# Optimization experiments

Measured on AMD Instinct MI355X. Metric: run time of the kernel, lower is better.

The kernel has to match this reference:

```python
import jax, jax.numpy as jnp
import numpy as np

EPS = 1e-5
R = 3


def _layernorm(x, gamma, beta):
    mu = jnp.mean(x, axis=-1, keepdims=True)
    var = jnp.mean(jnp.square(x - mu), axis=-1, keepdims=True)
    return (x - mu) * jax.lax.rsqrt(var + EPS) * gamma + beta


def setup_inputs() -> dict:
    key = jax.random.key(0)
    ks = jax.random.split(key, 16)
    N, C, H, W = 32, 256, 32, 32
    ic = C // 2
    L = H * W
    R2 = R * R
    d_attn = R2 * L        # 9216
    d_out = ic * L         # 131072
    return {
        "x": jax.random.normal(ks[0], (N, C, H, W), jnp.float32),
        "wq": jax.random.normal(ks[1], (ic, C), jnp.float32) / np.sqrt(C),
        "wk": jax.random.normal(ks[2], (ic, C), jnp.float32) / np.sqrt(C),
        "gamma1": jnp.ones((d_attn,), jnp.float32),
        "beta1": jnp.zeros((d_attn,), jnp.float32),
        "w1": jax.random.normal(ks[3], (C, d_attn), jnp.float32) / np.sqrt(d_attn),
        "b1": jnp.zeros((C,), jnp.float32),
        "w2": jax.random.normal(ks[4], (d_out, C), jnp.float32) / np.sqrt(C),
        "b2": jnp.zeros((d_out,), jnp.float32),
        "gamma2": jnp.ones((d_out,), jnp.float32),
        "beta2": jnp.zeros((d_out,), jnp.float32),
        "w_out": jax.random.normal(ks[5], (C, ic), jnp.float32) / np.sqrt(ic),
        "bn_gamma": jax.random.normal(ks[6], (C,), jnp.float32),
        "bn_beta": jax.random.normal(ks[7], (C,), jnp.float32),
        "bn_mean": jax.random.normal(ks[8], (C,), jnp.float32),
        "bn_var": jax.random.uniform(ks[9], (C,), jnp.float32, 0.5, 1.5),
    }


def reference(x, wq, wk, gamma1, beta1, w1, b1, w2, b2, gamma2, beta2,
              w_out, bn_gamma, bn_beta, bn_mean, bn_var):
    N, C, H, W = x.shape
    ic = wq.shape[0]
    L = H * W
    R2 = R * R
    pad = (R - 1) // 2

    # 1x1 convs == channel GEMMs
    q = jnp.einsum('nchw,oc->nohw', x, wq).reshape(N, ic, L)       # [N,ic,L]
    k = jnp.einsum('nchw,oc->nohw', x, wk)                          # [N,ic,H,W]

    # unfold: RxR local patches, torch channel-major ordering [ic, R2]
    kp = jnp.pad(k, ((0, 0), (0, 0), (pad, pad), (pad, pad)))
    patches = jnp.stack([kp[:, :, i:i + H, j:j + W]
                         for i in range(R) for j in range(R)], axis=-1)
    patches = patches.reshape(N, ic, L, R2)                         # [N,ic,L,R2]

    # local attention scores: q . k over channels at each spatial loc
    f = jnp.einsum('ncl,nclr->nlr', q, patches)                     # [N,L,R2]
    f = f.transpose(0, 2, 1).reshape(N, R2 * L)                     # [N, R2*L]

    # f = f + dropout(f) -> identity at inference => 2f
    f = f + f
    f = _layernorm(f, gamma1, beta1)

    # FFN
    h = jax.nn.relu(f @ w1.T + b1)                                  # [N,C]
    h = h @ w2.T + b2                                               # [N, ic*L]
    h = _layernorm(h, gamma2, beta2)
    y = h.reshape(N, ic, H, W)

    # output 1x1 conv + BatchNorm2d (inference mode)
    wy = jnp.einsum('nchw,oc->nohw', y, w_out)                      # [N,C,H,W]
    scale = (bn_gamma * jax.lax.rsqrt(bn_var + EPS))[None, :, None, None]
    wy = (wy - bn_mean[None, :, None, None]) * scale + bn_beta[None, :, None, None]
    return wy + x
```

## Files before the change

kernel.cpp:

```cpp
#include <hip/hip_runtime.h>

#define NN 32
#define CC 256
#define LL 1024
#define IC 128
#define R2 9
#define DA 9216
#define DOUT 131072
#define EPSF 1e-5f

typedef __attribute__((ext_vector_type(8))) short short8;
typedef __attribute__((ext_vector_type(4))) float f32x4;

__device__ __forceinline__ ushort bf_rne(float f) {
  union { float f; unsigned u; } v;
  v.f = f;
  unsigned u = v.u;
  u += 0x7FFF + ((u >> 16) & 1);
  return (ushort)(u >> 16);
}

__global__ __launch_bounds__(256) void k_xt(const float* __restrict__ x,
                                            ushort* __restrict__ xt) {
  int n = blockIdx.y;
  int l = blockIdx.x * 128 + (threadIdx.x & 127);
  int chalf = (threadIdx.x >> 7) * 128;
  const float* xn = x + ((size_t)n * CC) * LL;
  ushort* xr = xt + ((size_t)n * LL + l) * CC + chalf;
#pragma unroll 4
  for (int c4 = 0; c4 < 32; c4++) {
    float a = xn[(size_t)(chalf + c4 * 4 + 0) * LL + l];
    float b = xn[(size_t)(chalf + c4 * 4 + 1) * LL + l];
    float c = xn[(size_t)(chalf + c4 * 4 + 2) * LL + l];
    float d = xn[(size_t)(chalf + c4 * 4 + 3) * LL + l];
    ushort4 o;
    o.x = bf_rne(a); o.y = bf_rne(b); o.z = bf_rne(c); o.w = bf_rne(d);
    *(ushort4*)(xr + c4 * 4) = o;
  }
}

__global__ __launch_bounds__(256, 1) void k_qk(const ushort* __restrict__ xt,
                                               const float* __restrict__ wq,
                                               const float* __restrict__ wk,
                                               float* __restrict__ q,
                                               float* __restrict__ k) {
  int bx = blockIdx.x;
  int n = blockIdx.y;
  int mt = bx & 1, lt = bx >> 1;
  int l0 = lt * 256;
  int t = threadIdx.x;
  int lane = t & 63, wv = t >> 6;
  int m16 = lane & 15, kg = lane >> 4;
  const float* wrow = mt ? wk : wq;

  short8 a[2][8];
#pragma unroll
  for (int ms = 0; ms < 2; ms++)
#pragma unroll
    for (int kc = 0; kc < 8; kc++) {
      const float* ap =
          wrow + (size_t)(wv * 32 + ms * 16 + m16) * CC + kc * 32 + kg * 8;
      short8 v;
#pragma unroll
      for (int j = 0; j < 8; j++) v[j] = (short)bf_rne(ap[j]);
      a[ms][kc] = v;
    }

  f32x4 acc0[16], acc1[16];
#pragma unroll
  for (int i = 0; i < 16; i++) {
    acc0[i] = (f32x4){0.f, 0.f, 0.f, 0.f};
    acc1[i] = (f32x4){0.f, 0.f, 0.f, 0.f};
  }

  const ushort* xrow = xt + ((size_t)n * LL + l0 + m16) * CC + kg * 8;
#pragma unroll
  for (int kc = 0; kc < 8; kc++) {
#pragma unroll
    for (int ls = 0; ls < 16; ls++) {
      short8 b = *(const short8*)(xrow + (size_t)ls * 16 * CC + kc * 32);
      acc0[ls] =
          __builtin_amdgcn_mfma_f32_16x16x32_bf16(a[0][kc], b, acc0[ls], 0, 0, 0);
      acc1[ls] =
          __builtin_amdgcn_mfma_f32_16x16x32_bf16(a[1][kc], b, acc1[ls], 0, 0, 0);
    }
  }

  float* outp = (mt ? k : q) + (size_t)n * IC * LL;
  int mq = kg * 4;
#pragma unroll
  for (int ls = 0; ls < 16; ls++) {
    int col = l0 + ls * 16 + m16;
#pragma unroll
    for (int r = 0; r < 4; r++) {
      outp[(size_t)(wv * 32 + mq + r) * LL + col] = acc0[ls][r];
      outp[(size_t)(wv * 32 + 16 + mq + r) * LL + col] = acc1[ls][r];
    }
  }
}

__global__ __launch_bounds__(256) void k_attn(const float* __restrict__ q,
                                              const float* __restrict__ k,
                                              float* __restrict__ f2) {
  int n = blockIdx.x;
  int c0 = blockIdx.y * 32;
  int l = blockIdx.z * 256 + threadIdx.x;
  int h = l >> 5, w = l & 31;
  const float* qn = q + (size_t)n * IC * LL;
  const float* kn = k + (size_t)n * IC * LL;
  bool val[9];
  int off[9];
#pragma unroll
  for (int i = 0; i < 3; i++)
#pragma unroll
    for (int j = 0; j < 3; j++) {
      int r = i * 3 + j;
      int hh = h + i - 1, ww = w + j - 1;
      val[r] = (hh >= 0 && hh < 32 && ww >= 0 && ww < 32);
      off[r] = hh * 32 + ww;
    }
  float acc[9];
#pragma unroll
  for (int r = 0; r < 9; r++) acc[r] = 0.f;
#pragma unroll 4
  for (int cc = 0; cc < 32; cc++) {
    int c = c0 + cc;
    float qv = qn[c * LL + l];
    const float* kc = kn + c * LL;
#pragma unroll
    for (int r = 0; r < 9; r++) {
      float kv = val[r] ? kc[off[r]] : 0.f;
      acc[r] += qv * kv;
    }
  }
#pragma unroll
  for (int r = 0; r < 9; r++)
    atomicAdd(&f2[(size_t)n * DA + r * LL + l], 2.f * acc[r]);
}

__global__ __launch_bounds__(256) void k_ln1(float* __restrict__ f2,
                                             const float* __restrict__ g1,
                                             const float* __restrict__ b1) {
  int n = blockIdx.x, t = threadIdx.x;
  float* row = f2 + (size_t)n * DA;
  float4 v[9];
  float s = 0.f, ss = 0.f;
#pragma unroll
  for (int kk = 0; kk < 9; kk++) {
    v[kk] = ((const float4*)row)[t + kk * 256];
    s += v[kk].x + v[kk].y + v[kk].z + v[kk].w;
    ss += v[kk].x * v[kk].x + v[kk].y * v[kk].y + v[kk].z * v[kk].z +
          v[kk].w * v[kk].w;
  }
#pragma unroll
  for (int o = 32; o; o >>= 1) {
    s += __shfl_down(s, o);
    ss += __shfl_down(ss, o);
  }
  __shared__ float ps[4], pss[4], stats[2];
  int wid = t >> 6, lid = t & 63;
  if (lid == 0) { ps[wid] = s; pss[wid] = ss; }
  __syncthreads();
  if (t == 0) {
    float S = ps[0] + ps[1] + ps[2] + ps[3];
    float SS = pss[0] + pss[1] + pss[2] + pss[3];
    float mu = S / DA;
    float var = SS / DA - mu * mu;
    stats[0] = mu;
    stats[1] = rsqrtf(var + EPSF);
  }
  __syncthreads();
  float mu = stats[0], rs = stats[1];
#pragma unroll
  for (int kk = 0; kk < 9; kk++) {
    float4 g = ((const float4*)g1)[t + kk * 256];
    float4 b = ((const float4*)b1)[t + kk * 256];
    float4 o;
    o.x = (v[kk].x - mu) * rs * g.x + b.x;
    o.y = (v[kk].y - mu) * rs * g.y + b.y;
    o.z = (v[kk].z - mu) * rs * g.z + b.z;
    o.w = (v[kk].w - mu) * rs * g.w + b.w;
    ((float4*)row)[t + kk * 256] = o;
  }
}

__global__ __launch_bounds__(256) void k_ffn1(const float* __restrict__ fln,
                                              const float* __restrict__ w1,
                                              const float* __restrict__ b1,
                                              ushort* __restrict__ h1bf) {
  int o = blockIdx.x, nsb = blockIdx.y * 8, t = threadIdx.x;
  float acc[8];
#pragma unroll
  for (int i = 0; i < 8; i++) acc[i] = 0.f;
  const float4* w1r = (const float4*)(w1 + (size_t)o * DA);
  for (int kk = 0; kk < 9; kk++) {
    float4 wv = w1r[t + kk * 256];
#pragma unroll
    for (int i = 0; i < 8; i++) {
      float4 fv = ((const float4*)(fln + (size_t)(nsb + i) * DA))[t + kk * 256];
      acc[i] += wv.x * fv.x + wv.y * fv.y + wv.z * fv.z + wv.w * fv.w;
    }
  }
#pragma unroll
  for (int i = 0; i < 8; i++)
#pragma unroll
    for (int s = 32; s; s >>= 1) acc[i] += __shfl_down(acc[i], s);
  __shared__ float part[4][8];
  int wid = t >> 6, lid = t & 63;
  if (lid == 0) {
#pragma unroll
    for (int i = 0; i < 8; i++) part[wid][i] = acc[i];
  }
  __syncthreads();
  if (t < 8) {
    float sum = part[0][t] + part[1][t] + part[2][t] + part[3][t] + b1[o];
    h1bf[(size_t)(nsb + t) * CC + o] = bf_rne(fmaxf(sum, 0.f));
  }
}

__global__ __launch_bounds__(256, 3) void k_ffn2(
    const ushort* __restrict__ h1bf, const float* __restrict__ w2,
    const float* __restrict__ b2, float* __restrict__ h2,
    float* __restrict__ st_part) {
  __shared__ float bs[64];
  int t = threadIdx.x;
  int lane = t & 63, wv = t >> 6;
  int m16 = lane & 15, kg = lane >> 4;
  int j0 = blockIdx.x * 256 + wv * 64;
  if (t < 64) bs[t] = 0.f;

  short8 a[2][8];
#pragma unroll
  for (int m = 0; m < 2; m++)
#pragma unroll
    for (int kc = 0; kc < 8; kc++)
      a[m][kc] = *(const short8*)(h1bf + (size_t)(m * 16 + m16) * CC +
                                  kc * 32 + kg * 8);

  f32x4 acc[2][4];
#pragma unroll
  for (int m = 0; m < 2; m++)
#pragma unroll
    for (int n = 0; n < 4; n++) acc[m][n] = (f32x4){0.f, 0.f, 0.f, 0.f};

  int j[4];
#pragma unroll
  for (int n = 0; n < 4; n++) j[n] = j0 + n * 16 + m16;

#pragma unroll
  for (int kc = 0; kc < 8; kc++) {
    short8 bfrag[4];
#pragma unroll
    for (int n = 0; n < 4; n++) {
      const float* src = w2 + (size_t)j[n] * CC + kc * 32 + kg * 8;
      float4 lo = *(const float4*)src;
      float4 hi = *(const float4*)(src + 4);
      union { short8 s; ushort u[8]; } cv;
      cv.u[0] = bf_rne(lo.x); cv.u[1] = bf_rne(lo.y);
      cv.u[2] = bf_rne(lo.z); cv.u[3] = bf_rne(lo.w);
      cv.u[4] = bf_rne(hi.x); cv.u[5] = bf_rne(hi.y);
      cv.u[6] = bf_rne(hi.z); cv.u[7] = bf_rne(hi.w);
      bfrag[n] = cv.s;
    }
#pragma unroll
    for (int m = 0; m < 2; m++)
#pragma unroll
      for (int n = 0; n < 4; n++)
        acc[m][n] = __builtin_amdgcn_mfma_f32_16x16x32_bf16(a[m][kc], bfrag[n],
                                                            acc[m][n], 0, 0, 0);
  }
  __syncthreads();

  float b2v[4];
#pragma unroll
  for (int n = 0; n < 4; n++) b2v[n] = b2[j[n]];

  float s8[2][4], q8[2][4];
#pragma unroll
  for (int m = 0; m < 2; m++)
#pragma unroll
    for (int r = 0; r < 4; r++) { s8[m][r] = 0.f; q8[m][r] = 0.f; }
#pragma unroll
  for (int m = 0; m < 2; m++)
#pragma unroll
    for (int n = 0; n < 4; n++) {
#pragma unroll
      for (int r = 0; r < 4; r++) {
        float v = acc[m][n][r] + b2v[n];
        int row = m * 16 + kg * 4 + r;
        h2[(size_t)row * DOUT + j[n]] = v;
        s8[m][r] += v;
        q8[m][r] += v * v;
      }
    }
#pragma unroll
  for (int off = 8; off; off >>= 1)
#pragma unroll
    for (int m = 0; m < 2; m++)
#pragma unroll
      for (int r = 0; r < 4; r++) {
        s8[m][r] += __shfl_down(s8[m][r], off, 16);
        q8[m][r] += __shfl_down(q8[m][r], off, 16);
      }
  if (m16 == 0) {
#pragma unroll
    for (int m = 0; m < 2; m++)
#pragma unroll
      for (int r = 0; r < 4; r++) {
        int row = m * 16 + kg * 4 + r;
        atomicAdd(&bs[row], s8[m][r]);
        atomicAdd(&bs[32 + row], q8[m][r]);
      }
  }
  __syncthreads();
  if (t < 64) st_part[(size_t)blockIdx.x * 64 + t] = bs[t];
}

__global__ __launch_bounds__(256) void k_stat(const float* __restrict__ st_part,
                                              float* __restrict__ st) {
  int e = blockIdx.x;
  int t = threadIdx.x;
  float s = 0.f;
  for (int p = t; p < 512; p += 256) s += st_part[(size_t)p * 64 + e];
#pragma unroll
  for (int off = 32; off; off >>= 1) s += __shfl_down(s, off);
  __shared__ float ps[4];
  if ((t & 63) == 0) ps[t >> 6] = s;
  __syncthreads();
  if (t == 0) st[e] = ps[0] + ps[1] + ps[2] + ps[3];
}

__global__ __launch_bounds__(256) void k_out(
    const float* __restrict__ h2, const float* __restrict__ st,
    const float* __restrict__ g2, const float* __restrict__ b2,
    const float* __restrict__ w_out, const float* __restrict__ bn_g,
    const float* __restrict__ bn_b, const float* __restrict__ bn_m,
    const float* __restrict__ bn_v, const float* __restrict__ x,
    float* __restrict__ out) {
  __shared__ float wt[IC * 32];
  __shared__ float yt[16 * 256];
  int t = threadIdx.x;
  int l0 = blockIdx.x * 256;
  int Ob = blockIdx.y * 32;
  int n = blockIdx.z;
  for (int f = t; f < IC * 32; f += 256) {
    int Os = f & 31, o = f >> 5;
    wt[o * 32 + Os] = w_out[(size_t)(Ob + Os) * IC + o];
  }
  float mu = st[n] * (1.f / DOUT);
  float rs = rsqrtf(st[32 + n] * (1.f / DOUT) - mu * mu + EPSF);
  int lane = t & 63, wid = t >> 6;
  int Obase = wid * 8;
  int ll = lane * 4;
  float4 acc[8];
#pragma unroll
  for (int i = 0; i < 8; i++) acc[i] = make_float4(0.f, 0.f, 0.f, 0.f);

  for (int o0 = 0; o0 < IC; o0 += 16) {
    __syncthreads();
#pragma unroll
    for (int u = 0; u < 16; u++) {
      int d = (o0 + u) * LL + l0 + t;
      float yv = (h2[(size_t)n * DOUT + d] - mu) * rs * g2[d] + b2[d];
      yt[u * 256 + t] = yv;
    }
    __syncthreads();
#pragma unroll
    for (int oc = 0; oc < 16; oc++) {
      int o = o0 + oc;
      float4 w0 = *(const float4*)&wt[o * 32 + Obase];
      float4 w1v = *(const float4*)&wt[o * 32 + Obase + 4];
      float4 yv = *(const float4*)&yt[oc * 256 + ll];
#define FMA_O(wc, idx)                                                        \
  acc[idx].x += yv.x * (wc); acc[idx].y += yv.y * (wc);                       \
  acc[idx].z += yv.z * (wc); acc[idx].w += yv.w * (wc);
      FMA_O(w0.x, 0) FMA_O(w0.y, 1) FMA_O(w0.z, 2) FMA_O(w0.w, 3)
      FMA_O(w1v.x, 4) FMA_O(w1v.y, 5) FMA_O(w1v.z, 6) FMA_O(w1v.w, 7)
#undef FMA_O
    }
  }
#pragma unroll
  for (int i = 0; i < 8; i++) {
    int O = Ob + Obase + i;
    float sc = bn_g[O] * rsqrtf(bn_v[O] + EPSF);
    float sh = bn_b[O] - bn_m[O] * sc;
    size_t base = ((size_t)(n * CC + O)) * LL + l0 + ll;
    float4 xv = *(const float4*)(x + base);
    float4 r;
    r.x = acc[i].x * sc + sh + xv.x;
    r.y = acc[i].y * sc + sh + xv.y;
    r.z = acc[i].z * sc + sh + xv.z;
    r.w = acc[i].w * sc + sh + xv.w;
    *(float4*)(out + base) = r;
  }
}

extern "C" void kernel_launch(void* const* d_in, const int* in_sizes, int n_in,
                              void* d_out, int out_size, void* d_ws,
                              size_t ws_size, hipStream_t stream) {
  const float* x = (const float*)d_in[0];
  const float* wq = (const float*)d_in[1];
  const float* wk = (const float*)d_in[2];
  const float* gamma1 = (const float*)d_in[3];
  const float* beta1 = (const float*)d_in[4];
  const float* w1 = (const float*)d_in[5];
  const float* b1 = (const float*)d_in[6];
  const float* w2 = (const float*)d_in[7];
  const float* b2 = (const float*)d_in[8];
  const float* gamma2 = (const float*)d_in[9];
  const float* beta2 = (const float*)d_in[10];
  const float* w_out = (const float*)d_in[11];
  const float* bn_g = (const float*)d_in[12];
  const float* bn_b = (const float*)d_in[13];
  const float* bn_m = (const float*)d_in[14];
  const float* bn_v = (const float*)d_in[15];
  float* outp = (float*)d_out;
  float* ws = (float*)d_ws;

  float* qb = ws;
  float* kb = ws + 4194304;
  ushort* xtb = (ushort*)(ws + 8388608);
  float* fb = ws + 12582912;
  float* stp = ws + 12877824;
  ushort* h1bfb = (ushort*)(ws + 12877888);
  float* spart = ws + 12886080;
  float* h2b = qb;

  if (ws_size < 12951616ull * sizeof(float)) return;

  hipMemsetAsync(fb, 0, 294912 * sizeof(float), stream);
  k_xt<<<dim3(8, 32), 256, 0, stream>>>(x, xtb);
  k_qk<<<dim3(8, 32), 256, 0, stream>>>(xtb, wq, wk, qb, kb);
  k_attn<<<dim3(32, 4, 4), 256, 0, stream>>>(qb, kb, fb);
  k_ln1<<<dim3(32), 256, 0, stream>>>(fb, gamma1, beta1);
  k_ffn1<<<dim3(256, 4), 256, 0, stream>>>(fb, w1, b1, h1bfb);
  k_ffn2<<<dim3(512), 256, 0, stream>>>(h1bfb, w2, b2, h2b, spart);
  k_stat<<<dim3(64), 256, 0, stream>>>(spart, stp);
  k_out<<<dim3(4, 8, 32), 256, 0, stream>>>(h2b, stp, gamma2, beta2, w_out,
                                            bn_g, bn_b, bn_m, bn_v, x, outp);
}
```

Before: 411.9 us.

## Fuse x transpose into QK GEMM, move output conv to MFMA, drop stat kernel

Removes the separate x transpose/convert kernel. The QK GEMM now converts x into LDS itself and reads weights that a new small kernel pre-converts to bf16. The output 1x1 conv moves from fp32 FMA to bf16 MFMA with y staged in LDS, and the ffn2 statistics reduce through global atomics instead of a separate reduction kernel. ffn2 also software-prefetches the w2 fragments one k-step ahead. This saves a launch and the intermediate xt traffic, at the cost of bf16 rounding in the output conv and nondeterministic atomic summation order.

```diff
diff --git a/kernel.cpp b/kernel.cpp
--- a/kernel.cpp
+++ b/kernel.cpp
@@ -4,7 +4,6 @@
 #define CC 256
 #define LL 1024
 #define IC 128
-#define R2 9
 #define DA 9216
 #define DOUT 131072
 #define EPSF 1e-5f
@@ -20,82 +19,91 @@
   return (ushort)(u >> 16);
 }
 
-__global__ __launch_bounds__(256) void k_xt(const float* __restrict__ x,
-                                            ushort* __restrict__ xt) {
+__global__ __launch_bounds__(256) void k_wcvt(const float* __restrict__ wq,
+                                              const float* __restrict__ wk,
+                                              const float* __restrict__ wo,
+                                              ushort* __restrict__ wqkbf,
+                                              ushort* __restrict__ wobf) {
+  int idx = (blockIdx.x * 256 + threadIdx.x) * 4;
+  float4 v;
+  if (idx < 32768) v = *(const float4*)(wq + idx);
+  else if (idx < 65536) v = *(const float4*)(wk + idx - 32768);
+  else v = *(const float4*)(wo + idx - 65536);
+  ushort4 o;
+  o.x = bf_rne(v.x); o.y = bf_rne(v.y); o.z = bf_rne(v.z); o.w = bf_rne(v.w);
+  if (idx < 65536) *(ushort4*)(wqkbf + idx) = o;
+  else *(ushort4*)(wobf + idx - 65536) = o;
+}
+
+__global__ __launch_bounds__(256, 4) void k_qkx(const float* __restrict__ x,
+                                                const ushort* __restrict__ wqkbf,
+                                                float* __restrict__ q,
+                                                float* __restrict__ k) {
+  __shared__ ushort xl[64 * 264];
+  int t = threadIdx.x;
   int n = blockIdx.y;
-  int l = blockIdx.x * 128 + (threadIdx.x & 127);
-  int chalf = (threadIdx.x >> 7) * 128;
-  const float* xn = x + ((size_t)n * CC) * LL;
-  ushort* xr = xt + ((size_t)n * LL + l) * CC + chalf;
-#pragma unroll 4
-  for (int c4 = 0; c4 < 32; c4++) {
-    float a = xn[(size_t)(chalf + c4 * 4 + 0) * LL + l];
-    float b = xn[(size_t)(chalf + c4 * 4 + 1) * LL + l];
-    float c = xn[(size_t)(chalf + c4 * 4 + 2) * LL + l];
-    float d = xn[(size_t)(chalf + c4 * 4 + 3) * LL + l];
-    ushort4 o;
-    o.x = bf_rne(a); o.y = bf_rne(b); o.z = bf_rne(c); o.w = bf_rne(d);
-    *(ushort4*)(xr + c4 * 4) = o;
-  }
-}
-
-__global__ __launch_bounds__(256, 1) void k_qk(const ushort* __restrict__ xt,
-                                               const float* __restrict__ wq,
-                                               const float* __restrict__ wk,
-                                               float* __restrict__ q,
-                                               float* __restrict__ k) {
-  int bx = blockIdx.x;
-  int n = blockIdx.y;
-  int mt = bx & 1, lt = bx >> 1;
-  int l0 = lt * 256;
-  int t = threadIdx.x;
+  int l0 = blockIdx.x * 64;
   int lane = t & 63, wv = t >> 6;
   int m16 = lane & 15, kg = lane >> 4;
-  const float* wrow = mt ? wk : wq;
-
-  short8 a[2][8];
-#pragma unroll
-  for (int ms = 0; ms < 2; ms++)
-#pragma unroll
-    for (int kc = 0; kc < 8; kc++) {
-      const float* ap =
-          wrow + (size_t)(wv * 32 + ms * 16 + m16) * CC + kc * 32 + kg * 8;
-      short8 v;
-#pragma unroll
-      for (int j = 0; j < 8; j++) v[j] = (short)bf_rne(ap[j]);
-      a[ms][kc] = v;
-    }
-
-  f32x4 acc0[16], acc1[16];
-#pragma unroll
-  for (int i = 0; i < 16; i++) {
-    acc0[i] = (f32x4){0.f, 0.f, 0.f, 0.f};
-    acc1[i] = (f32x4){0.f, 0.f, 0.f, 0.f};
-  }
-
-  const ushort* xrow = xt + ((size_t)n * LL + l0 + m16) * CC + kg * 8;
+
+  {
+    int l = t & 63, g = t >> 6;
+    const float* xn = x + ((size_t)n * CC) * LL + l0 + l;
+#pragma unroll
+    for (int i = 0; i < 8; i++) {
+      int c8 = (i * 4 + g) * 8;
+      union { short8 s; ushort u[8]; } p;
+#pragma unroll
+      for (int j = 0; j < 8; j++) p.u[j] = bf_rne(xn[(size_t)(c8 + j) * LL]);
+      *(short8*)&xl[l * 264 + c8] = p.s;
+    }
+  }
+  __syncthreads();
+
+  f32x4 acc[2][2][4];
+#pragma unroll
+  for (int mt = 0; mt < 2; mt++)
+#pragma unroll
+    for (int ms = 0; ms < 2; ms++)
+#pragma unroll
+      for (int ls = 0; ls < 4; ls++) acc[mt][ms][ls] = (f32x4){0.f, 0.f, 0.f, 0.f};
+
 #pragma unroll
   for (int kc = 0; kc < 8; kc++) {
-#pragma unroll
-    for (int ls = 0; ls < 16; ls++) {
-      short8 b = *(const short8*)(xrow + (size_t)ls * 16 * CC + kc * 32);
-      acc0[ls] =
-          __builtin_amdgcn_mfma_f32_16x16x32_bf16(a[0][kc], b, acc0[ls], 0, 0, 0);
-      acc1[ls] =
-          __builtin_amdgcn_mfma_f32_16x16x32_bf16(a[1][kc], b, acc1[ls], 0, 0, 0);
-    }
-  }
-
-  float* outp = (mt ? k : q) + (size_t)n * IC * LL;
-  int mq = kg * 4;
-#pragma unroll
-  for (int ls = 0; ls < 16; ls++) {
-    int col = l0 + ls * 16 + m16;
-#pragma unroll
-    for (int r = 0; r < 4; r++) {
-      outp[(size_t)(wv * 32 + mq + r) * LL + col] = acc0[ls][r];
-      outp[(size_t)(wv * 32 + 16 + mq + r) * LL + col] = acc1[ls][r];
-    }
+    short8 a[2][2];
+#pragma unroll
+    for (int mt = 0; mt < 2; mt++)
+#pragma unroll
+      for (int ms = 0; ms < 2; ms++)
+        a[mt][ms] = *(const short8*)(wqkbf +
+            (((mt * 128 + wv * 32 + ms * 16 + m16) << 8) + kc * 32 + kg * 8));
+#pragma unroll
+    for (int ls = 0; ls < 4; ls++) {
+      short8 b = *(const short8*)&xl[(ls * 16 + m16) * 264 + kc * 32 + kg * 8];
+      acc[0][0][ls] =
+          __builtin_amdgcn_mfma_f32_16x16x32_bf16(a[0][0], b, acc[0][0][ls], 0, 0, 0);
+      acc[0][1][ls] =
+          __builtin_amdgcn_mfma_f32_16x16x32_bf16(a[0][1], b, acc[0][1][ls], 0, 0, 0);
+      acc[1][0][ls] =
+          __builtin_amdgcn_mfma_f32_16x16x32_bf16(a[1][0], b, acc[1][0][ls], 0, 0, 0);
+      acc[1][1][ls] =
+          __builtin_amdgcn_mfma_f32_16x16x32_bf16(a[1][1], b, acc[1][1][ls], 0, 0, 0);
+    }
+  }
+
+#pragma unroll
+  for (int mt = 0; mt < 2; mt++) {
+    float* outp = (mt ? k : q) + (size_t)n * IC * LL;
+#pragma unroll
+    for (int ms = 0; ms < 2; ms++)
+#pragma unroll
+      for (int ls = 0; ls < 4; ls++) {
+        int col = l0 + ls * 16 + m16;
+#pragma unroll
+        for (int r = 0; r < 4; r++)
+          outp[(size_t)(wv * 32 + ms * 16 + kg * 4 + r) * LL + col] =
+              acc[mt][ms][ls][r];
+      }
   }
 }
 
@@ -221,7 +229,7 @@
 __global__ __launch_bounds__(256, 3) void k_ffn2(
     const ushort* __restrict__ h1bf, const float* __restrict__ w2,
     const float* __restrict__ b2, float* __restrict__ h2,
-    float* __restrict__ st_part) {
+    float* __restrict__ st) {
   __shared__ float bs[64];
   int t = threadIdx.x;
   int lane = t & 63, wv = t >> 6;
@@ -229,66 +237,74 @@
   int j0 = blockIdx.x * 256 + wv * 64;
   if (t < 64) bs[t] = 0.f;
 
-  short8 a[2][8];
+  int j[4];
+#pragma unroll
+  for (int nn = 0; nn < 4; nn++) j[nn] = j0 + nn * 16 + m16;
+
+  f32x4 acc[2][4];
 #pragma unroll
   for (int m = 0; m < 2; m++)
 #pragma unroll
-    for (int kc = 0; kc < 8; kc++)
-      a[m][kc] = *(const short8*)(h1bf + (size_t)(m * 16 + m16) * CC +
-                                  kc * 32 + kg * 8);
-
-  f32x4 acc[2][4];
+    for (int nn = 0; nn < 4; nn++) acc[m][nn] = (f32x4){0.f, 0.f, 0.f, 0.f};
+
+  float4 lo[4], hi[4];
+#pragma unroll
+  for (int nn = 0; nn < 4; nn++) {
+    const float* src = w2 + (size_t)j[nn] * CC + kg * 8;
+    lo[nn] = *(const float4*)src;
+    hi[nn] = *(const float4*)(src + 4);
+  }
+
+#pragma unroll
+  for (int kc = 0; kc < 8; kc++) {
+    short8 a0 = *(const short8*)(h1bf + m16 * CC + kc * 32 + kg * 8);
+    short8 a1 = *(const short8*)(h1bf + (16 + m16) * CC + kc * 32 + kg * 8);
+    short8 bf[4];
+#pragma unroll
+    for (int nn = 0; nn < 4; nn++) {
+      union { short8 s; ushort u[8]; } cv;
+      cv.u[0] = bf_rne(lo[nn].x); cv.u[1] = bf_rne(lo[nn].y);
+      cv.u[2] = bf_rne(lo[nn].z); cv.u[3] = bf_rne(lo[nn].w);
+      cv.u[4] = bf_rne(hi[nn].x); cv.u[5] = bf_rne(hi[nn].y);
+      cv.u[6] = bf_rne(hi[nn].z); cv.u[7] = bf_rne(hi[nn].w);
+      bf[nn] = cv.s;
+    }
+    if (kc < 7) {
+#pragma unroll
+      for (int nn = 0; nn < 4; nn++) {
+        const float* src = w2 + (size_t)j[nn] * CC + (kc + 1) * 32 + kg * 8;
+        lo[nn] = *(const float4*)src;
+        hi[nn] = *(const float4*)(src + 4);
+      }
+    }
+#pragma unroll
+    for (int nn = 0; nn < 4; nn++) {
+      acc[0][nn] =
+          __builtin_amdgcn_mfma_f32_16x16x32_bf16(a0, bf[nn], acc[0][nn], 0, 0, 0);
+      acc[1][nn] =
+          __builtin_amdgcn_mfma_f32_16x16x32_bf16(a1, bf[nn], acc[1][nn], 0, 0, 0);
+    }
+  }
+  __syncthreads();
+
+  float b2v[4];
+#pragma unroll
+  for (int nn = 0; nn < 4; nn++) b2v[nn] = b2[j[nn]];
+
+  float s8[2][4], q8[2][4];
 #pragma unroll
   for (int m = 0; m < 2; m++)
 #pragma unroll
-    for (int n = 0; n < 4; n++) acc[m][n] = (f32x4){0.f, 0.f, 0.f, 0.f};
-
-  int j[4];
-#pragma unroll
-  for (int n = 0; n < 4; n++) j[n] = j0 + n * 16 + m16;
-
-#pragma unroll
-  for (int kc = 0; kc < 8; kc++) {
-    short8 bfrag[4];
-#pragma unroll
-    for (int n = 0; n < 4; n++) {
-      const float* src = w2 + (size_t)j[n] * CC + kc * 32 + kg * 8;
-      float4 lo = *(const float4*)src;
-      float4 hi = *(const float4*)(src + 4);
-      union { short8 s; ushort u[8]; } cv;
-      cv.u[0] = bf_rne(lo.x); cv.u[1] = bf_rne(lo.y);
-      cv.u[2] = bf_rne(lo.z); cv.u[3] = bf_rne(lo.w);
-      cv.u[4] = bf_rne(hi.x); cv.u[5] = bf_rne(hi.y);
-      cv.u[6] = bf_rne(hi.z); cv.u[7] = bf_rne(hi.w);
-      bfrag[n] = cv.s;
-    }
-#pragma unroll
-    for (int m = 0; m < 2; m++)
-#pragma unroll
-      for (int n = 0; n < 4; n++)
-        acc[m][n] = __builtin_amdgcn_mfma_f32_16x16x32_bf16(a[m][kc], bfrag[n],
-                                                            acc[m][n], 0, 0, 0);
-  }
-  __syncthreads();
-
-  float b2v[4];
-#pragma unroll
-  for (int n = 0; n < 4; n++) b2v[n] = b2[j[n]];
-
-  float s8[2][4], q8[2][4];
+    for (int r = 0; r < 4; r++) { s8[m][r] = 0.f; q8[m][r] = 0.f; }
 #pragma unroll
   for (int m = 0; m < 2; m++)
 #pragma unroll
-    for (int r = 0; r < 4; r++) { s8[m][r] = 0.f; q8[m][r] = 0.f; }
-#pragma unroll
-  for (int m = 0; m < 2; m++)
-#pragma unroll
-    for (int n = 0; n < 4; n++) {
+    for (int nn = 0; nn < 4; nn++) {
 #pragma unroll
       for (int r = 0; r < 4; r++) {
-        float v = acc[m][n][r] + b2v[n];
+        float v = acc[m][nn][r] + b2v[nn];
         int row = m * 16 + kg * 4 + r;
-        h2[(size_t)row * DOUT + j[n]] = v;
+        h2[(size_t)row * DOUT + j[nn]] = v;
         s8[m][r] += v;
         q8[m][r] += v * v;
       }
@@ -313,86 +329,80 @@
       }
   }
   __syncthreads();
-  if (t < 64) st_part[(size_t)blockIdx.x * 64 + t] = bs[t];
-}
-
-__global__ __launch_bounds__(256) void k_stat(const float* __restrict__ st_part,
-                                              float* __restrict__ st) {
-  int e = blockIdx.x;
-  int t = threadIdx.x;
-  float s = 0.f;
-  for (int p = t; p < 512; p += 256) s += st_part[(size_t)p * 64 + e];
-#pragma unroll
-  for (int off = 32; off; off >>= 1) s += __shfl_down(s, off);
-  __shared__ float ps[4];
-  if ((t & 63) == 0) ps[t >> 6] = s;
-  __syncthreads();
-  if (t == 0) st[e] = ps[0] + ps[1] + ps[2] + ps[3];
-}
-
-__global__ __launch_bounds__(256) void k_out(
+  if (t < 64) atomicAdd(&st[t], bs[t]);
+}
+
+__global__ __launch_bounds__(256, 2) void k_out(
     const float* __restrict__ h2, const float* __restrict__ st,
     const float* __restrict__ g2, const float* __restrict__ b2,
-    const float* __restrict__ w_out, const float* __restrict__ bn_g,
+    const ushort* __restrict__ wobf, const float* __restrict__ bn_g,
     const float* __restrict__ bn_b, const float* __restrict__ bn_m,
     const float* __restrict__ bn_v, const float* __restrict__ x,
     float* __restrict__ out) {
-  __shared__ float wt[IC * 32];
-  __shared__ float yt[16 * 256];
+  __shared__ ushort yl[64 * 136];
   int t = threadIdx.x;
-  int l0 = blockIdx.x * 256;
-  int Ob = blockIdx.y * 32;
-  int n = blockIdx.z;
-  for (int f = t; f < IC * 32; f += 256) {
-    int Os = f & 31, o = f >> 5;
-    wt[o * 32 + Os] = w_out[(size_t)(Ob + Os) * IC + o];
-  }
+  int n = blockIdx.y;
+  int l0 = blockIdx.x * 64;
   float mu = st[n] * (1.f / DOUT);
   float rs = rsqrtf(st[32 + n] * (1.f / DOUT) - mu * mu + EPSF);
-  int lane = t & 63, wid = t >> 6;
-  int Obase = wid * 8;
-  int ll = lane * 4;
-  float4 acc[8];
-#pragma unroll
-  for (int i = 0; i < 8; i++) acc[i] = make_float4(0.f, 0.f, 0.f, 0.f);
-
-  for (int o0 = 0; o0 < IC; o0 += 16) {
-    __syncthreads();
-#pragma unroll
-    for (int u = 0; u < 16; u++) {
-      int d = (o0 + u) * LL + l0 + t;
-      float yv = (h2[(size_t)n * DOUT + d] - mu) * rs * g2[d] + b2[d];
-      yt[u * 256 + t] = yv;
-    }
-    __syncthreads();
-#pragma unroll
-    for (int oc = 0; oc < 16; oc++) {
-      int o = o0 + oc;
-      float4 w0 = *(const float4*)&wt[o * 32 + Obase];
-      float4 w1v = *(const float4*)&wt[o * 32 + Obase + 4];
-      float4 yv = *(const float4*)&yt[oc * 256 + ll];
-#define FMA_O(wc, idx)                                                        \
-  acc[idx].x += yv.x * (wc); acc[idx].y += yv.y * (wc);                       \
-  acc[idx].z += yv.z * (wc); acc[idx].w += yv.w * (wc);
-      FMA_O(w0.x, 0) FMA_O(w0.y, 1) FMA_O(w0.z, 2) FMA_O(w0.w, 3)
-      FMA_O(w1v.x, 4) FMA_O(w1v.y, 5) FMA_O(w1v.z, 6) FMA_O(w1v.w, 7)
-#undef FMA_O
-    }
-  }
-#pragma unroll
-  for (int i = 0; i < 8; i++) {
-    int O = Ob + Obase + i;
-    float sc = bn_g[O] * rsqrtf(bn_v[O] + EPSF);
-    float sh = bn_b[O] - bn_m[O] * sc;
-    size_t base = ((size_t)(n * CC + O)) * LL + l0 + ll;
-    float4 xv = *(const float4*)(x + base);
-    float4 r;
-    r.x = acc[i].x * sc + sh + xv.x;
-    r.y = acc[i].y * sc + sh + xv.y;
-    r.z = acc[i].z * sc + sh + xv.z;
-    r.w = acc[i].w * sc + sh + xv.w;
-    *(float4*)(out + base) = r;
-  }
+
+  {
+    int l = t & 63, og = t >> 6;
+    const float* h2n = h2 + (size_t)n * DOUT;
+#pragma unroll
+    for (int i = 0; i < 4; i++) {
+      int o8 = (i * 4 + og) * 8;
+      union { short8 s; ushort u[8]; } p;
+#pragma unroll
+      for (int jj = 0; jj < 8; jj++) {
+        int d = (o8 + jj) * LL + l0 + l;
+        float yv = (h2n[d] - mu) * rs * g2[d] + b2[d];
+        p.u[jj] = bf_rne(yv);
+      }
+      *(short8*)&yl[l * 136 + o8] = p.s;
+    }
+  }
+  __syncthreads();
+
+  int lane = t & 63, wv = t >> 6;
+  int m16 = lane & 15, kg = lane >> 4;
+  f32x4 acc[4][4];
+#pragma unroll
+  for (int ms = 0; ms < 4; ms++)
+#pragma unroll
+    for (int ls = 0; ls < 4; ls++) acc[ms][ls] = (f32x4){0.f, 0.f, 0.f, 0.f};
+
+#pragma unroll
+  for (int kc = 0; kc < 4; kc++) {
+    short8 a[4];
+#pragma unroll
+    for (int ms = 0; ms < 4; ms++)
+      a[ms] = *(const short8*)(wobf +
+          (((wv * 64 + ms * 16 + m16) << 7) + kc * 32 + kg * 8));
+#pragma unroll
+    for (int ls = 0; ls < 4; ls++) {
+      short8 b = *(const short8*)&yl[(ls * 16 + m16) * 136 + kc * 32 + kg * 8];
+#pragma unroll
+      for (int ms = 0; ms < 4; ms++)
+        acc[ms][ls] =
+            __builtin_amdgcn_mfma_f32_16x16x32_bf16(a[ms], b, acc[ms][ls], 0, 0, 0);
+    }
+  }
+
+#pragma unroll
+  for (int ms = 0; ms < 4; ms++)
+#pragma unroll
+    for (int r = 0; r < 4; r++) {
+      int O = wv * 64 + ms * 16 + kg * 4 + r;
+      float sc = bn_g[O] * rsqrtf(bn_v[O] + EPSF);
+      float sh = bn_b[O] - bn_m[O] * sc;
+#pragma unroll
+      for (int ls = 0; ls < 4; ls++) {
+        int col = l0 + ls * 16 + m16;
+        size_t base = ((size_t)(n * CC + O)) * LL + col;
+        out[base] = acc[ms][ls][r] * sc + sh + x[base];
+      }
+    }
 }
 
 extern "C" void kernel_launch(void* const* d_in, const int* in_sizes, int n_in,
@@ -419,23 +429,22 @@
 
   float* qb = ws;
   float* kb = ws + 4194304;
-  ushort* xtb = (ushort*)(ws + 8388608);
-  float* fb = ws + 12582912;
-  float* stp = ws + 12877824;
-  ushort* h1bfb = (ushort*)(ws + 12877888);
-  float* spart = ws + 12886080;
+  float* fb = ws + 8388608;
+  float* stb = ws + 8683520;
+  ushort* h1bfb = (ushort*)(ws + 8683584);
+  ushort* wqkbfb = (ushort*)(ws + 8687680);
+  ushort* wobfb = (ushort*)(ws + 8720448);
   float* h2b = qb;
 
-  if (ws_size < 12951616ull * sizeof(float)) return;
-
-  hipMemsetAsync(fb, 0, 294912 * sizeof(float), stream);
-  k_xt<<<dim3(8, 32), 256, 0, stream>>>(x, xtb);
-  k_qk<<<dim3(8, 32), 256, 0, stream>>>(xtb, wq, wk, qb, kb);
+  if (ws_size < 8736832ull * sizeof(float)) return;
+
+  hipMemsetAsync(fb, 0, (294912 + 64) * sizeof(float), stream);
+  k_wcvt<<<dim3(96), 256, 0, stream>>>(wq, wk, w_out, wqkbfb, wobfb);
+  k_qkx<<<dim3(16, 32), 256, 0, stream>>>(x, wqkbfb, qb, kb);
   k_attn<<<dim3(32, 4, 4), 256, 0, stream>>>(qb, kb, fb);
   k_ln1<<<dim3(32), 256, 0, stream>>>(fb, gamma1, beta1);
   k_ffn1<<<dim3(256, 4), 256, 0, stream>>>(fb, w1, b1, h1bfb);
-  k_ffn2<<<dim3(512), 256, 0, stream>>>(h1bfb, w2, b2, h2b, spart);
-  k_stat<<<dim3(64), 256, 0, stream>>>(spart, stp);
-  k_out<<<dim3(4, 8, 32), 256, 0, stream>>>(h2b, stp, gamma2, beta2, w_out,
-                                            bn_g, bn_b, bn_m, bn_v, x, outp);
-}
+  k_ffn2<<<dim3(512), 256, 0, stream>>>(h1bfb, w2, b2, h2b, stb);
+  k_out<<<dim3(16, 32), 256, 0, stream>>>(h2b, stb, gamma2, beta2, wobfb,
+                                          bn_g, bn_b, bn_m, bn_v, x, outp);
+}
```

New measurement: 333.5 us. 1.23x faster.
